# Kernel tuning notes

Hardware: AMD Instinct MI355X
Metric: run time of the kernel (lower is better)

The kernel has to match this reference:

```python
import jax, jax.numpy as jnp
import numpy as np

N = 50000   # nodes (= batch_size = num_e)
D = 256     # d_dim = n_hidden
E = 320000  # edges (first half 'in' direction, second half 'out'/inverse)
R = 400     # relation types (incl. inverses)


def setup_inputs() -> dict:
    key = jax.random.key(0)
    ks = jax.random.split(key, 12)
    s = 0.05  # weight scale so tanh stays in linear-ish range
    w = lambda k, shp: jax.random.normal(k, shp, jnp.float32) * s
    return {
        "emb": jax.random.normal(ks[0], (N, D), jnp.float32),
        "edge_index": jax.random.randint(ks[1], (2, E), 0, N),
        "edge_type": jax.random.randint(ks[2], (E,), 0, R),
        "rel1": w(ks[3], (R, D)),
        "W_in1": w(ks[4], (D, D)),
        "W_out1": w(ks[5], (D, D)),
        "W_loop1": w(ks[6], (D, D)),
        "b1": jnp.zeros((D,), jnp.float32),
        "rel2": w(ks[7], (R, D)),
        "W_in2": w(ks[8], (D, D)),
        "W_out2": w(ks[9], (D, D)),
        "W_loop2": w(ks[10], (D, D)),
        "b2": jnp.zeros((D,), jnp.float32),
        "res": jnp.array([0.1], jnp.float32),
        "mu_w": w(ks[11], (D, D)),
        "mu_b": jnp.zeros((D,), jnp.float32),
        "num_nodes": N,
    }


def _mgcn_conv(x, edge_index, edge_type, rel, W_in, W_out, W_loop, b, n):
    """Relational conv: gather -> compose with relation emb -> direction-split
    linear transform -> degree-normalized scatter-add -> self-loop -> tanh."""
    src, dst = edge_index[0], edge_index[1]
    e = edge_index.shape[1]
    half = e // 2
    m = x[src] * rel[edge_type]                                   # [E, D] compose ('mult')
    m = jnp.concatenate([m[:half] @ W_in, m[half:] @ W_out], 0)    # direction-specific transform
    deg = jax.ops.segment_sum(jnp.ones((e,), x.dtype), dst, num_segments=n)
    norm = 1.0 / jnp.maximum(deg, 1.0)                             # 1/in-degree
    agg = jax.ops.segment_sum(m * norm[dst][:, None], dst, num_segments=n)
    return jnp.tanh(agg + x @ W_loop + b)


def reference(emb, edge_index, edge_type,
              rel1, W_in1, W_out1, W_loop1, b1,
              rel2, W_in2, W_out2, W_loop2, b2,
              res, mu_w, mu_b, num_nodes):
    # forward_base with p.res=True, core_layer=2, dropout in eval mode (identity)
    h = emb + res * _mgcn_conv(emb, edge_index, edge_type, rel1, W_in1, W_out1, W_loop1, b1, num_nodes)
    h = h + res * _mgcn_conv(h, edge_index, edge_type, rel2, W_in2, W_out2, W_loop2, b2, num_nodes)
    # drift head f(t, y) = mu(forward_base(y))
    return h @ mu_w + mu_b
```

## Files before the change

kernel.cpp:

```cpp
#include <hip/hip_runtime.h>
#include <hip/hip_bf16.h>
#include <cstdint>
#include <cstddef>


typedef short bf16x8 __attribute__((ext_vector_type(8)));
typedef float f32x4  __attribute__((ext_vector_type(4)));

__device__ __forceinline__ float b2f(unsigned short u) {
    union { unsigned u32; float f; } c; c.u32 = ((unsigned)u) << 16; return c.f;
}
__device__ __forceinline__ unsigned short f2b(float f) {
    union { float f; unsigned u; } c; c.f = f;
    unsigned r = c.u + 0x7FFFu + ((c.u >> 16) & 1u);
    return (unsigned short)(r >> 16);
}
__device__ __forceinline__ float ftanh(float x) {
    float e = __expf(2.0f * x);
    return 1.0f - __fdividef(2.0f, e + 1.0f);
}


__global__ void k_hist(const int* __restrict__ dst, int* __restrict__ cnt, int E) {
    int i = blockIdx.x * blockDim.x + threadIdx.x;
    if (i < E) atomicAdd(&cnt[dst[i]], 1);
}

__global__ void k_norm(const int* __restrict__ cnt, float* __restrict__ norm, int N) {
    int i = blockIdx.x * blockDim.x + threadIdx.x;
    if (i < N) norm[i] = 1.0f / fmaxf((float)cnt[i], 1.0f);
}

__global__ void k_scan1(const int* __restrict__ cnt, int* __restrict__ part,
                        int* __restrict__ bsum, int N) {
    __shared__ int s[256];
    int i = blockIdx.x * 256 + threadIdx.x;
    int v = (i < N) ? cnt[i] : 0;
    s[threadIdx.x] = v; __syncthreads();
    #pragma unroll
    for (int o = 1; o < 256; o <<= 1) {
        int t = (threadIdx.x >= o) ? s[threadIdx.x - o] : 0;
        __syncthreads();
        s[threadIdx.x] += t;
        __syncthreads();
    }
    if (i < N) part[i] = s[threadIdx.x] - v;
    if (threadIdx.x == 255) bsum[blockIdx.x] = s[255];
}

__global__ void k_scan2(int* __restrict__ bsum, int nb) {
    __shared__ int s[256];
    int v = (threadIdx.x < nb) ? bsum[threadIdx.x] : 0;
    s[threadIdx.x] = v; __syncthreads();
    #pragma unroll
    for (int o = 1; o < 256; o <<= 1) {
        int t = (threadIdx.x >= o) ? s[threadIdx.x - o] : 0;
        __syncthreads();
        s[threadIdx.x] += t;
        __syncthreads();
    }
    if (threadIdx.x < nb) bsum[threadIdx.x] = s[threadIdx.x] - v;
}

__global__ void k_scan3(const int* __restrict__ part, const int* __restrict__ bsum,
                        int* __restrict__ rowptr, int* __restrict__ cursor, int N, int E) {
    int i = blockIdx.x * 256 + threadIdx.x;
    if (i < N) {
        int r = part[i] + bsum[blockIdx.x];
        rowptr[i] = r; cursor[i] = r;
    }
    if (i == 0) rowptr[N] = E;
}

__global__ void k_scatter(const int* __restrict__ src, const int* __restrict__ dst,
                          const int* __restrict__ et, int* __restrict__ cursor,
                          unsigned* __restrict__ erec, int E, int halfE) {
    int e = blockIdx.x * blockDim.x + threadIdx.x;
    if (e < E) {
        int d = dst[e];
        int pos = atomicAdd(&cursor[d], 1);
        unsigned rec = (unsigned)src[e] | ((unsigned)et[e] << 16)
                     | ((e >= halfE) ? 0x80000000u : 0u);
        erec[pos] = rec;
    }
}


__global__ void k_cvt3(const float* __restrict__ s0, unsigned short* __restrict__ d0, long n0,
                       const float* __restrict__ s1, unsigned short* __restrict__ d1, long n1,
                       const float* __restrict__ s2, unsigned short* __restrict__ d2, long n2) {
    long i = (long)blockIdx.x * blockDim.x + threadIdx.x;
    const float* s; unsigned short* d; long j = i;
    if (j < n0) { s = s0; d = d0; }
    else {
        j -= n0;
        if (j < n1) { s = s1; d = d1; }
        else { j -= n1; if (j >= n2) return; s = s2; d = d2; }
    }
    float4 v = ((const float4*)s)[j];
    ushort4 o;
    o.x = f2b(v.x); o.y = f2b(v.y); o.z = f2b(v.z); o.w = f2b(v.w);
    ((ushort4*)d)[j] = o;
}

__global__ void k_wfrag7(const float* __restrict__ w0, const float* __restrict__ w1,
                         const float* __restrict__ w2, const float* __restrict__ w3,
                         const float* __restrict__ w4, const float* __restrict__ w5,
                         const float* __restrict__ w6, unsigned short* __restrict__ out) {
    int o = blockIdx.x * 256 + threadIdx.x;
    int mi = o >> 16;
    int r  = o & 65535;
    const float* W = (mi == 0) ? w0 : (mi == 1) ? w1 : (mi == 2) ? w2 :
                     (mi == 3) ? w3 : (mi == 4) ? w4 : (mi == 5) ? w5 : w6;
    int j  = r & 7;
    int l  = (r >> 3) & 63;
    int nn = (r >> 9) & 15;
    int kg = r >> 13;
    int k = kg * 32 + (l >> 4) * 8 + j;
    int n = nn * 16 + (l & 15);
    out[o] = f2b(W[k * 256 + n]);
}


__global__ __launch_bounds__(256)
void k_agg(const unsigned short* __restrict__ xb, const unsigned short* __restrict__ relb,
           const int* __restrict__ rowptr, const unsigned* __restrict__ erec,
           const float* __restrict__ norm,
           unsigned short* __restrict__ sIn, unsigned short* __restrict__ sOut,
           int N, int D)
{
    const int w = threadIdx.x >> 6, l = threadIdx.x & 63;
    const int v = blockIdx.x * 4 + w;
    if (v >= N) return;
    const int rs = rowptr[v], re = rowptr[v + 1];
    const float nm = norm[v];

    float ai0 = 0, ai1 = 0, ai2 = 0, ai3 = 0;
    float ao0 = 0, ao1 = 0, ao2 = 0, ao3 = 0;

    unsigned c0 = (rs     < re) ? erec[rs]     : 0u;
    unsigned c1 = (rs + 1 < re) ? erec[rs + 1] : 0u;
    unsigned c2 = (rs + 2 < re) ? erec[rs + 2] : 0u;
    unsigned c3 = (rs + 3 < re) ? erec[rs + 3] : 0u;
    int i = rs;
    while (i + 4 <= re) {
        unsigned m0 = (i + 4 < re) ? erec[i + 4] : 0u;
        unsigned m1 = (i + 5 < re) ? erec[i + 5] : 0u;
        unsigned m2 = (i + 6 < re) ? erec[i + 6] : 0u;
        unsigned m3 = (i + 7 < re) ? erec[i + 7] : 0u;
        ushort4 x0 = *(const ushort4*)(xb   + (size_t)(c0 & 0xffff) * D + l * 4);
        ushort4 r0 = *(const ushort4*)(relb + (size_t)((c0 >> 16) & 0x7fff) * D + l * 4);
        ushort4 x1 = *(const ushort4*)(xb   + (size_t)(c1 & 0xffff) * D + l * 4);
        ushort4 r1 = *(const ushort4*)(relb + (size_t)((c1 >> 16) & 0x7fff) * D + l * 4);
        ushort4 x2 = *(const ushort4*)(xb   + (size_t)(c2 & 0xffff) * D + l * 4);
        ushort4 r2 = *(const ushort4*)(relb + (size_t)((c2 >> 16) & 0x7fff) * D + l * 4);
        ushort4 x3 = *(const ushort4*)(xb   + (size_t)(c3 & 0xffff) * D + l * 4);
        ushort4 r3 = *(const ushort4*)(relb + (size_t)((c3 >> 16) & 0x7fff) * D + l * 4);
        float p0, p1, p2, p3;
        p0 = b2f(x0.x)*b2f(r0.x); p1 = b2f(x0.y)*b2f(r0.y);
        p2 = b2f(x0.z)*b2f(r0.z); p3 = b2f(x0.w)*b2f(r0.w);
        if (c0 >> 31) { ao0 += p0; ao1 += p1; ao2 += p2; ao3 += p3; }
        else          { ai0 += p0; ai1 += p1; ai2 += p2; ai3 += p3; }
        p0 = b2f(x1.x)*b2f(r1.x); p1 = b2f(x1.y)*b2f(r1.y);
        p2 = b2f(x1.z)*b2f(r1.z); p3 = b2f(x1.w)*b2f(r1.w);
        if (c1 >> 31) { ao0 += p0; ao1 += p1; ao2 += p2; ao3 += p3; }
        else          { ai0 += p0; ai1 += p1; ai2 += p2; ai3 += p3; }
        p0 = b2f(x2.x)*b2f(r2.x); p1 = b2f(x2.y)*b2f(r2.y);
        p2 = b2f(x2.z)*b2f(r2.z); p3 = b2f(x2.w)*b2f(r2.w);
        if (c2 >> 31) { ao0 += p0; ao1 += p1; ao2 += p2; ao3 += p3; }
        else          { ai0 += p0; ai1 += p1; ai2 += p2; ai3 += p3; }
        p0 = b2f(x3.x)*b2f(r3.x); p1 = b2f(x3.y)*b2f(r3.y);
        p2 = b2f(x3.z)*b2f(r3.z); p3 = b2f(x3.w)*b2f(r3.w);
        if (c3 >> 31) { ao0 += p0; ao1 += p1; ao2 += p2; ao3 += p3; }
        else          { ai0 += p0; ai1 += p1; ai2 += p2; ai3 += p3; }
        c0 = m0; c1 = m1; c2 = m2; c3 = m3; i += 4;
    }
    #pragma unroll
    for (int j = 0; j < 3; ++j) {
        if (i + j < re) {
            unsigned cur = (j == 0) ? c0 : (j == 1) ? c1 : c2;
            ushort4 x0 = *(const ushort4*)(xb   + (size_t)(cur & 0xffff) * D + l * 4);
            ushort4 r0 = *(const ushort4*)(relb + (size_t)((cur >> 16) & 0x7fff) * D + l * 4);
            float p0 = b2f(x0.x)*b2f(r0.x), p1 = b2f(x0.y)*b2f(r0.y);
            float p2 = b2f(x0.z)*b2f(r0.z), p3 = b2f(x0.w)*b2f(r0.w);
            if (cur >> 31) { ao0 += p0; ao1 += p1; ao2 += p2; ao3 += p3; }
            else           { ai0 += p0; ai1 += p1; ai2 += p2; ai3 += p3; }
        }
    }

    ushort4 oi, oo;
    oi.x = f2b(ai0 * nm); oi.y = f2b(ai1 * nm); oi.z = f2b(ai2 * nm); oi.w = f2b(ai3 * nm);
    oo.x = f2b(ao0 * nm); oo.y = f2b(ao1 * nm); oo.z = f2b(ao2 * nm); oo.w = f2b(ao3 * nm);
    *(ushort4*)(sIn  + (size_t)v * D + l * 4) = oi;
    *(ushort4*)(sOut + (size_t)v * D + l * 4) = oo;
}


#define GIT(S, AtC, AtN, Rw0, Rw1, Rl0, Rl1, Bc, Bn)                            \
  do {                                                                          \
    if ((S) + 1 < 12) {                                                         \
      *(uint4*)(&AtN[wo0]) = Rw0;                                               \
      *(uint4*)(&AtN[wo1]) = Rw1;                                               \
    }                                                                           \
    if ((S) + 1 < 12) {                                                         \
      const int pn_ = ((S) + 1) >> 2, cbn_ = ((S) + 1) & 3;                     \
      const unsigned short* __restrict__ Wn_ = Wf + (size_t)pn_ * 65536;        \
      _Pragma("unroll")                                                         \
      for (int kk_ = 0; kk_ < 2; ++kk_) {                                       \
        _Pragma("unroll")                                                       \
        for (int n_ = 0; n_ < 4; ++n_) {                                        \
          Bn[kk_ * 4 + n_] = *(const bf16x8*)(Wn_ +                             \
              ((((cbn_ * 2 + kk_) * 16 + (w * 4 + n_)) * 64 + l) * 8));         \
        }                                                                       \
      }                                                                         \
    }                                                                           \
    {                                                                           \
      const int cb_ = (S) & 3;                                                  \
      _Pragma("unroll")                                                         \
      for (int kk_ = 0; kk_ < 2; ++kk_) {                                       \
        (void)cb_;                                                              \
        bf16x8 a_[4];                                                           \
        _Pragma("unroll")                                                       \
        for (int m_ = 0; m_ < 4; ++m_) {                                        \
          int rm_ = 16 * m_ + lr;                                               \
          int ch_ = (kk_ * 4 + lq) ^ (rm_ & 7);                                 \
          a_[m_] = *(const bf16x8*)(&AtC[rm_ * 64 + ch_ * 8]);                  \
        }                                                                       \
        _Pragma("unroll")                                                       \
        for (int m_ = 0; m_ < 4; ++m_) {                                        \
          _Pragma("unroll")                                                     \
          for (int n_ = 0; n_ < 4; ++n_) {                                      \
            acc[m_][n_] = __builtin_amdgcn_mfma_f32_16x16x32_bf16(a_[m_], Bc[kk_ * 4 + n_], acc[m_][n_], 0, 0, 0); \
          }                                                                     \
        }                                                                       \
      }                                                                         \
    }                                                                           \
    if ((S) + 3 < 12) {                                                         \
      const int p3_ = ((S) + 3) >> 2, cb3_ = ((S) + 3) & 3;                     \
      const unsigned short* ap_ = (p3_ == 0) ? a0 : ((p3_ == 1) ? a1 : a2);     \
      Rl0 = *(const uint4*)(ap_ + g0 + cb3_ * 64);                              \
      Rl1 = *(const uint4*)(ap_ + g1 + cb3_ * 64);                              \
    }                                                                           \
    asm volatile("s_waitcnt lgkmcnt(0)" ::: "memory");                          \
    __builtin_amdgcn_sched_barrier(0);                                          \
    __builtin_amdgcn_s_barrier();                                               \
    __builtin_amdgcn_sched_barrier(0);                                          \
  } while (0)

template <bool HEAD>
__global__ __launch_bounds__(256, 2)
void k_gemm(const unsigned short* __restrict__ a0,
            const unsigned short* __restrict__ a1,
            const unsigned short* __restrict__ a2,
            const unsigned short* __restrict__ Wf,
            const float* __restrict__ bias,
            const float* __restrict__ resPtr,
            const unsigned short* __restrict__ WfMu,
            const float* __restrict__ mub,
            float* __restrict__ outF,
            unsigned short* __restrict__ outB,
            int N, int D)
{
    __shared__ unsigned short lds[HEAD ? 16384 : 8192];
    unsigned short* At0 = lds;
    unsigned short* At1 = lds + 4096;

    const int t = threadIdx.x;
    const int rBase = blockIdx.x * 64;

    const int w  = t >> 6;
    const int l  = t & 63;
    const int lr = l & 15;
    const int lq = l >> 4;

    const int rS0 = t >> 3;
    const int rS1 = rS0 + 32;
    const int cS  = t & 7;
    const int wo0 = rS0 * 64 + ((cS ^ (rS0 & 7)) * 8);
    const int wo1 = rS1 * 64 + ((cS ^ (rS1 & 7)) * 8);
    const size_t g0 = (size_t)min(rBase + rS0, N - 1) * D + cS * 8;
    const size_t g1 = (size_t)min(rBase + rS1, N - 1) * D + cS * 8;

    f32x4 acc[4][4] = {};
    uint4 Ra0, Ra1, Rb0, Rb1, Rc0, Rc1;
    bf16x8 B0[8], B1[8];

    Ra0 = *(const uint4*)(a0 + g0);
    Ra1 = *(const uint4*)(a0 + g1);
    Rb0 = *(const uint4*)(a0 + g0 + 64);
    Rb1 = *(const uint4*)(a0 + g1 + 64);
    Rc0 = *(const uint4*)(a0 + g0 + 128);
    Rc1 = *(const uint4*)(a0 + g1 + 128);
    #pragma unroll
    for (int kk = 0; kk < 2; ++kk) {
        #pragma unroll
        for (int n = 0; n < 4; ++n)
            B0[kk * 4 + n] = *(const bf16x8*)(Wf + (((kk * 16 + (w * 4 + n)) * 64 + l) * 8));
    }
    *(uint4*)(&At0[wo0]) = Ra0;
    *(uint4*)(&At0[wo1]) = Ra1;
    asm volatile("s_waitcnt lgkmcnt(0)" ::: "memory");
    __builtin_amdgcn_sched_barrier(0);
    __builtin_amdgcn_s_barrier();
    __builtin_amdgcn_sched_barrier(0);

    GIT(0,  At0, At1, Rb0, Rb1, Ra0, Ra1, B0, B1);
    GIT(1,  At1, At0, Rc0, Rc1, Rb0, Rb1, B1, B0);
    GIT(2,  At0, At1, Ra0, Ra1, Rc0, Rc1, B0, B1);
    GIT(3,  At1, At0, Rb0, Rb1, Ra0, Ra1, B1, B0);
    GIT(4,  At0, At1, Rc0, Rc1, Rb0, Rb1, B0, B1);
    GIT(5,  At1, At0, Ra0, Ra1, Rc0, Rc1, B1, B0);
    GIT(6,  At0, At1, Rb0, Rb1, Ra0, Ra1, B0, B1);
    GIT(7,  At1, At0, Rc0, Rc1, Rb0, Rb1, B1, B0);
    GIT(8,  At0, At1, Ra0, Ra1, Rc0, Rc1, B0, B1);
    GIT(9,  At1, At0, Rb0, Rb1, Ra0, Ra1, B1, B0);
    GIT(10, At0, At1, Rc0, Rc1, Rb0, Rb1, B0, B1);
    GIT(11, At1, At0, Ra0, Ra1, Rc0, Rc1, B1, B0);

    const int rb4 = lq * 4;
    const float resv = resPtr[0];

    if (!HEAD) {
        unsigned short* C = lds;
        #pragma unroll
        for (int half = 0; half < 2; ++half) {
            if ((w >> 1) == half) {
                #pragma unroll
                for (int m = 0; m < 4; ++m) {
                    #pragma unroll
                    for (int i = 0; i < 4; ++i) {
                        int r6 = 16 * m + rb4 + i;
                        #pragma unroll
                        for (int n = 0; n < 4; ++n) {
                            int cH = (w & 1) * 64 + lr + 16 * n;
                            float v = acc[m][n][i] + bias[half * 128 + cH];
                            C[r6 * 128 + cH] = f2b(resv * ftanh(v));
                        }
                    }
                }
            }
            __syncthreads();
            #pragma unroll
            for (int ii = 0; ii < 4; ++ii) {
                int g   = ii * 256 + t;
                int r   = g >> 4;
                int cc  = g & 15;
                int row = rBase + r;
                if (row < N) {
                    bf16x8 sv = *(const bf16x8*)(&C[r * 128 + cc * 8]);
                    const unsigned short* ar = a0 + (size_t)row * D + half * 128 + cc * 8;
                    uint4 av = *(const uint4*)ar;
                    unsigned aw[4] = { av.x, av.y, av.z, av.w };
                    unsigned ow[4];
                    #pragma unroll
                    for (int p = 0; p < 4; ++p) {
                        float h0 = b2f((unsigned short)(aw[p] & 0xffff)) + b2f((unsigned short)sv[2 * p]);
                        float h1 = b2f((unsigned short)(aw[p] >> 16))    + b2f((unsigned short)sv[2 * p + 1]);
                        ow[p] = (unsigned)f2b(h0) | ((unsigned)f2b(h1) << 16);
                    }
                    *(uint4*)(outB + (size_t)row * D + half * 128 + cc * 8) =
                        make_uint4(ow[0], ow[1], ow[2], ow[3]);
                }
            }
            __syncthreads();
        }
    } else {
        #pragma unroll
        for (int m = 0; m < 4; ++m) {
            #pragma unroll
            for (int i = 0; i < 4; ++i) {
                int row = rBase + 16 * m + rb4 + i;
                if (row < N) {
                    size_t base = (size_t)row * D + w * 64 + lr;
                    int r6 = 16 * m + rb4 + i;
                    #pragma unroll
                    for (int n = 0; n < 4; ++n) {
                        int   c = w * 64 + lr + 16 * n;
                        float v = acc[m][n][i] + bias[c];
                        float h = b2f(a0[base + 16 * n]) + resv * ftanh(v);
                        lds[r6 * 256 + (c ^ ((r6 & 7) << 3))] = f2b(h);
                    }
                }
            }
        }
        __syncthreads();
        #pragma unroll
        for (int m = 0; m < 4; ++m) {
            #pragma unroll
            for (int n = 0; n < 4; ++n)
                acc[m][n] = (f32x4){0.f, 0.f, 0.f, 0.f};
        }

        #pragma unroll
        for (int s2 = 0; s2 < 4; ++s2) {
            #pragma unroll
            for (int kk = 0; kk < 2; ++kk) {
                const int kg = s2 * 2 + kk;
                bf16x8 a_[4], b_[4];
                #pragma unroll
                for (int m = 0; m < 4; ++m) {
                    int rm = 16 * m + lr;
                    int ch = (s2 * 8 + kk * 4 + lq) ^ (rm & 7);
                    a_[m] = *(const bf16x8*)(&lds[rm * 256 + ch * 8]);
                }
                #pragma unroll
                for (int n = 0; n < 4; ++n)
                    b_[n] = *(const bf16x8*)(WfMu + (((kg * 16 + (w * 4 + n)) * 64 + l) * 8));
                #pragma unroll
                for (int m = 0; m < 4; ++m) {
                    #pragma unroll
                    for (int n = 0; n < 4; ++n)
                        acc[m][n] = __builtin_amdgcn_mfma_f32_16x16x32_bf16(a_[m], b_[n], acc[m][n], 0, 0, 0);
                }
            }
        }

        __syncthreads();
        float* Cf = (float*)lds;
        #pragma unroll
        for (int half = 0; half < 2; ++half) {
            if ((w >> 1) == half) {
                #pragma unroll
                for (int m = 0; m < 4; ++m) {
                    #pragma unroll
                    for (int i = 0; i < 4; ++i) {
                        int r6 = 16 * m + rb4 + i;
                        #pragma unroll
                        for (int n = 0; n < 4; ++n) {
                            int cH = (w & 1) * 64 + lr + 16 * n;
                            Cf[r6 * 128 + cH] = acc[m][n][i] + mub[half * 128 + cH];
                        }
                    }
                }
            }
            __syncthreads();
            #pragma unroll
            for (int ii = 0; ii < 8; ++ii) {
                int g   = ii * 256 + t;
                int r   = g >> 5;
                int cc  = g & 31;
                int row = rBase + r;
                if (row < N) {
                    *(float4*)(outF + (size_t)row * D + half * 128 + cc * 4) =
                        *(const float4*)(&Cf[r * 128 + cc * 4]);
                }
            }
            __syncthreads();
        }
    }
}


extern "C" void kernel_launch(void* const* d_in, const int* in_sizes, int n_in,
                              void* d_out, int out_size, void* d_ws, size_t ws_size,
                              hipStream_t stream)
{
    const float* emb  = (const float*)d_in[0];
    const int*   ei   = (const int*)  d_in[1];
    const int*   et   = (const int*)  d_in[2];
    const float* rel1 = (const float*)d_in[3];
    const float* Wi1  = (const float*)d_in[4];
    const float* Wo1  = (const float*)d_in[5];
    const float* Wl1  = (const float*)d_in[6];
    const float* b1   = (const float*)d_in[7];
    const float* rel2 = (const float*)d_in[8];
    const float* Wi2  = (const float*)d_in[9];
    const float* Wo2  = (const float*)d_in[10];
    const float* Wl2  = (const float*)d_in[11];
    const float* b2   = (const float*)d_in[12];
    const float* res  = (const float*)d_in[13];
    const float* muw  = (const float*)d_in[14];
    const float* mub  = (const float*)d_in[15];

    const int D = in_sizes[7];
    const int N = in_sizes[0] / D;
    const int E = in_sizes[2];
    const int R = in_sizes[3] / D;
    const int halfE = E / 2;
    const int* srcA = ei;
    const int* dstA = ei + E;
    const size_t DD = (size_t)D * D;

    char* ws = (char*)d_ws;
    size_t off = 0;
    auto alloc = [&](size_t bytes) -> char* {
        char* p = ws + off; off += (bytes + 255) & ~(size_t)255; return p;
    };
    const int nb1 = (N + 255) / 256;

    float*          norm   = (float*)          alloc((size_t)N * 4);
    int*            cnt    = (int*)            alloc((size_t)N * 4);
    int*            rowptr = (int*)            alloc((size_t)(N + 1) * 4);
    int*            cursor = (int*)            alloc((size_t)N * 4);
    int*            part   = (int*)            alloc((size_t)N * 4);
    int*            bsum   = (int*)            alloc(1024);
    unsigned*       erec   = (unsigned*)       alloc((size_t)E * 4);
    unsigned short* xb     = (unsigned short*) alloc((size_t)N * D * 2);
    unsigned short* h1b    = (unsigned short*) alloc((size_t)N * D * 2);
    unsigned short* sIn    = (unsigned short*) alloc((size_t)N * D * 2);
    unsigned short* sOut   = (unsigned short*) alloc((size_t)N * D * 2);
    unsigned short* r1b    = (unsigned short*) alloc((size_t)R * D * 2);
    unsigned short* r2b    = (unsigned short*) alloc((size_t)R * D * 2);
    unsigned short* fAll   = (unsigned short*) alloc(7 * DD * 2);
    if (off > ws_size) return;

    unsigned short* fW1 = fAll;
    unsigned short* fW2 = fAll + 3 * DD;
    unsigned short* fMu = fAll + 6 * DD;

    hipMemsetAsync(cnt, 0, (size_t)N * 4, stream);
    k_hist   <<<(E + 255) / 256, 256, 0, stream>>>(dstA, cnt, E);
    k_norm   <<<nb1, 256, 0, stream>>>(cnt, norm, N);
    k_scan1  <<<nb1, 256, 0, stream>>>(cnt, part, bsum, N);
    k_scan2  <<<1,   256, 0, stream>>>(bsum, nb1);
    k_scan3  <<<nb1, 256, 0, stream>>>(part, bsum, rowptr, cursor, N, E);
    k_scatter<<<(E + 255) / 256, 256, 0, stream>>>(srcA, dstA, et, cursor, erec, E, halfE);

    long nd4 = (long)N * D / 4, rd4 = (long)R * D / 4;
    long tot4 = nd4 + 2 * rd4;
    k_cvt3<<<(int)((tot4 + 255) / 256), 256, 0, stream>>>(
        emb, xb, nd4, rel1, r1b, rd4, rel2, r2b, rd4);
    k_wfrag7<<<(int)(7 * DD / 256), 256, 0, stream>>>(
        Wl1, Wi1, Wo1, Wl2, Wi2, Wo2, muw, fAll);

    const int AB = (N + 3) / 4;
    const int NB = (N + 63) / 64;

    k_agg<<<AB, 256, 0, stream>>>(xb, r1b, rowptr, erec, norm, sIn, sOut, N, D);
    k_gemm<false><<<NB, 256, 0, stream>>>(xb, sIn, sOut, fW1, b1, res,
                                          nullptr, nullptr, nullptr, h1b, N, D);

    k_agg<<<AB, 256, 0, stream>>>(h1b, r2b, rowptr, erec, norm, sIn, sOut, N, D);
    k_gemm<true><<<NB, 256, 0, stream>>>(h1b, sIn, sOut, fW2, b2, res,
                                         fMu, mub, (float*)d_out, nullptr, N, D);
}
```

Measured before the change: 229.1 us.

## Add per-wave 64x64 tiled layer-1 GEMM kernel with register-prefetched LDS double buffering

Replaces the first-layer fused GEMM with a new kernel in which each wave owns its own LDS double buffer for the A tiles. Loads are prefetched two stages ahead into registers, and the whole 64-row by 256-column output is computed per block in a single 12-step pass. The epilogue writes tanh results through LDS in two halves and adds the residual input. This avoids block-wide barriers in the main loop, at the cost of more registers and redundant A-tile loads across waves.

Result: slower. 239.3 us (+4.4%).

```diff
diff --git a/kernel.cpp b/kernel.cpp
--- a/kernel.cpp
+++ b/kernel.cpp
@@ -193,6 +193,136 @@
     oo.x = f2b(ao0 * nm); oo.y = f2b(ao1 * nm); oo.z = f2b(ao2 * nm); oo.w = f2b(ao3 * nm);
     *(ushort4*)(sIn  + (size_t)v * D + l * 4) = oi;
     *(ushort4*)(sOut + (size_t)v * D + l * 4) = oo;
+}
+
+
+__global__ __launch_bounds__(256, 2)
+void k_gemmW(const unsigned short* __restrict__ a0,
+             const unsigned short* __restrict__ a1,
+             const unsigned short* __restrict__ a2,
+             const unsigned short* __restrict__ Wf,
+             const float* __restrict__ bias,
+             const float* __restrict__ resPtr,
+             unsigned short* __restrict__ outB,
+             int N, int D)
+{
+    __shared__ unsigned short lds[4][2][4096];
+
+    const int t = threadIdx.x;
+    const int rBase = blockIdx.x * 64;
+    const int w  = t >> 6;
+    const int l  = t & 63;
+    const int lr = l & 15;
+    const int lq = l >> 4;
+
+    size_t gRow[8];
+    #pragma unroll
+    for (int j = 0; j < 8; ++j)
+        gRow[j] = (size_t)min(rBase + j * 8 + (l >> 3), N - 1) * 256 + (l & 7) * 8;
+    const int woBase = (l >> 3) * 64 + (((l & 7) ^ (l >> 3)) * 8);
+
+    f32x4 acc[4][4] = {};
+    uint4 Rg[8];
+
+    #pragma unroll
+    for (int j = 0; j < 8; ++j)
+        Rg[j] = *(const uint4*)(a0 + gRow[j]);
+    #pragma unroll
+    for (int j = 0; j < 8; ++j)
+        *(uint4*)(&lds[w][0][woBase + j * 512]) = Rg[j];
+    #pragma unroll
+    for (int j = 0; j < 8; ++j)
+        Rg[j] = *(const uint4*)(a0 + gRow[j] + 64);
+
+    #pragma unroll
+    for (int s = 0; s < 12; ++s) {
+        const unsigned short* __restrict__ At = lds[w][s & 1];
+        const int p = s >> 2, cb = s & 3;
+        const unsigned short* __restrict__ Wp = Wf + (size_t)p * 65536;
+
+        if (s + 1 < 12) {
+            unsigned short* An = &lds[w][(s + 1) & 1][0];
+            #pragma unroll
+            for (int j = 0; j < 8; ++j)
+                *(uint4*)(&An[woBase + j * 512]) = Rg[j];
+        }
+        if (s + 2 < 12) {
+            const int p2 = (s + 2) >> 2, cb2 = (s + 2) & 3;
+            const unsigned short* ap = (p2 == 0) ? a0 : ((p2 == 1) ? a1 : a2);
+            #pragma unroll
+            for (int j = 0; j < 8; ++j)
+                Rg[j] = *(const uint4*)(ap + gRow[j] + cb2 * 64);
+        }
+        (void)cb;
+
+        #pragma unroll
+        for (int kk = 0; kk < 2; ++kk) {
+            const int kg = cb * 2 + kk;
+            bf16x8 a_[4], b_[4];
+            #pragma unroll
+            for (int m = 0; m < 4; ++m) {
+                int rm = 16 * m + lr;
+                int ch = (kk * 4 + lq) ^ (rm & 7);
+                a_[m] = *(const bf16x8*)(&At[rm * 64 + ch * 8]);
+            }
+            #pragma unroll
+            for (int n = 0; n < 4; ++n)
+                b_[n] = *(const bf16x8*)(Wp + (((kg * 16 + (w * 4 + n)) * 64 + l) * 8));
+            #pragma unroll
+            for (int m = 0; m < 4; ++m) {
+                #pragma unroll
+                for (int n = 0; n < 4; ++n)
+                    acc[m][n] = __builtin_amdgcn_mfma_f32_16x16x32_bf16(a_[m], b_[n], acc[m][n], 0, 0, 0);
+            }
+        }
+    }
+
+    const int rb4 = lq * 4;
+    const float resv = resPtr[0];
+    unsigned short* C = (unsigned short*)lds;
+    __syncthreads();
+    #pragma unroll
+    for (int half = 0; half < 2; ++half) {
+        if (half) __syncthreads();
+        if ((w >> 1) == half) {
+            #pragma unroll
+            for (int m = 0; m < 4; ++m) {
+                #pragma unroll
+                for (int i = 0; i < 4; ++i) {
+                    int r6 = 16 * m + rb4 + i;
+                    #pragma unroll
+                    for (int n = 0; n < 4; ++n) {
+                        int cH = (w & 1) * 64 + lr + 16 * n;
+                        float v = acc[m][n][i] + bias[half * 128 + cH];
+                        C[r6 * 128 + cH] = f2b(resv * ftanh(v));
+                    }
+                }
+            }
+        }
+        __syncthreads();
+        #pragma unroll
+        for (int ii = 0; ii < 4; ++ii) {
+            int g   = ii * 256 + t;
+            int r   = g >> 4;
+            int cc  = g & 15;
+            int row = rBase + r;
+            if (row < N) {
+                bf16x8 sv = *(const bf16x8*)(&C[r * 128 + cc * 8]);
+                const unsigned short* ar = a0 + (size_t)row * D + half * 128 + cc * 8;
+                uint4 av = *(const uint4*)ar;
+                unsigned aw[4] = { av.x, av.y, av.z, av.w };
+                unsigned ow[4];
+                #pragma unroll
+                for (int p = 0; p < 4; ++p) {
+                    float h0 = b2f((unsigned short)(aw[p] & 0xffff)) + b2f((unsigned short)sv[2 * p]);
+                    float h1 = b2f((unsigned short)(aw[p] >> 16))    + b2f((unsigned short)sv[2 * p + 1]);
+                    ow[p] = (unsigned)f2b(h0) | ((unsigned)f2b(h1) << 16);
+                }
+                *(uint4*)(outB + (size_t)row * D + half * 128 + cc * 8) =
+                    make_uint4(ow[0], ow[1], ow[2], ow[3]);
+            }
+        }
+    }
 }
 
 
@@ -527,8 +657,7 @@
     const int NB = (N + 63) / 64;
 
     k_agg<<<AB, 256, 0, stream>>>(xb, r1b, rowptr, erec, norm, sIn, sOut, N, D);
-    k_gemm<false><<<NB, 256, 0, stream>>>(xb, sIn, sOut, fW1, b1, res,
-                                          nullptr, nullptr, nullptr, h1b, N, D);
+    k_gemmW<<<NB, 256, 0, stream>>>(xb, sIn, sOut, fW1, b1, res, h1b, N, D);
 
     k_agg<<<AB, 256, 0, stream>>>(h1b, r2b, rowptr, erec, norm, sIn, sOut, N, D);
     k_gemm<true><<<NB, 256, 0, stream>>>(h1b, sIn, sOut, fW2, b2, res,
```
